# Performance work log

Measured on AMD Instinct MI355X. Metric: run time of the kernel, lower is better.

## Reference

```python
import jax, jax.numpy as jnp
import numpy as np

B, T, D, H = 4, 2048, 1024, 16
HD = D // H

def setup_inputs() -> dict:
    key = jax.random.key(0)
    ks = jax.random.split(key, 5)
    s = 0.02
    return {
        "x": jax.random.normal(ks[0], (B, T, D), dtype=jnp.float32),
        "w_qkv": jax.random.normal(ks[1], (D, 3 * D), dtype=jnp.float32) * s,
        "b_qkv": jax.random.normal(ks[2], (3 * D,), dtype=jnp.float32) * s,
        "w_proj": jax.random.normal(ks[3], (D, D), dtype=jnp.float32) * s,
        "b_proj": jax.random.normal(ks[4], (D,), dtype=jnp.float32) * s,
    }

def reference(x, w_qkv, b_qkv, w_proj, b_proj):
    b, t, c = x.shape
    h, hd = H, HD
    scale = hd ** -0.5
    qkv = x @ w_qkv + b_qkv                       # [B,T,3D]
    qkv = qkv.reshape(b, t, 3, h, hd)
    q, k, v = qkv[:, :, 0], qkv[:, :, 1], qkv[:, :, 2]   # [B,T,H,HD]
    # scores [B,H,T,T]
    att = jnp.einsum('bqhd,bkhd->bhqk', q, k) * scale
    causal = jnp.tril(jnp.ones((t, t), dtype=bool))
    att = jnp.where(causal[None, None], att, -jnp.inf)
    w = jax.nn.softmax(att, axis=-1)
    out = jnp.einsum('bhqk,bkhd->bqhd', w, v).reshape(b, t, c)
    return out @ w_proj + b_proj
```

## Files before the change

### kernel.cpp

```cpp
#include <hip/hip_runtime.h>
#include <hip/hip_bf16.h>
#include <cstdint>

#define BB 4
#define TT 2048
#define DD 1024
#define HH 16
#define HD 64
#define MM (BB*TT)
#define NQKV (3*DD)
#define QSCALE 0.18033688f
#define NQT 16

typedef __bf16 bf16;
typedef __bf16 bf16x8 __attribute__((ext_vector_type(8)));
typedef float f32x4 __attribute__((ext_vector_type(4)));

#define AS1 __attribute__((address_space(1)))
#define AS3 __attribute__((address_space(3)))

__device__ __forceinline__ void gload_lds16(const void* g, void* l) {
  __builtin_amdgcn_global_load_lds((const AS1 uint32_t*)g, (AS3 uint32_t*)l, 16, 0, 0);
}

__global__ void k_cvt_x(const float* __restrict__ in, bf16* __restrict__ out) {
  int i = blockIdx.x * blockDim.x + threadIdx.x;
  float4 v = ((const float4*)in)[i];
  ushort4 o;
  o.x = __builtin_bit_cast(unsigned short, (bf16)v.x);
  o.y = __builtin_bit_cast(unsigned short, (bf16)v.y);
  o.z = __builtin_bit_cast(unsigned short, (bf16)v.z);
  o.w = __builtin_bit_cast(unsigned short, (bf16)v.w);
  ((ushort4*)out)[i] = o;
}

__global__ void k_transpose_w(const float* __restrict__ in, bf16* __restrict__ out,
                              int R, int C) {
  __shared__ float tile[32][33];
  const int c0 = blockIdx.x * 32, r0 = blockIdx.y * 32;
  const int tx = threadIdx.x & 31, ty = threadIdx.x >> 5;
#pragma unroll
  for (int i = 0; i < 32; i += 8)
    tile[ty + i][tx] = in[(long)(r0 + ty + i) * C + c0 + tx];
  __syncthreads();
#pragma unroll
  for (int i = 0; i < 32; i += 8)
    out[(long)(c0 + ty + i) * R + r0 + tx] = (bf16)tile[tx][ty + i];
}

__global__ void k_transpose_v(const bf16* __restrict__ V, bf16* __restrict__ Vt) {
  __shared__ bf16 tile[64][65];
  const int bh = blockIdx.z;
  const int t0 = blockIdx.x * 64;
  const bf16* src = V + (long)bh * TT * HD;
  bf16* dst = Vt + (long)bh * HD * TT;
  const int tx = threadIdx.x & 63, ty = threadIdx.x >> 6;
#pragma unroll
  for (int i = 0; i < 64; i += 4)
    tile[ty + i][tx] = src[(long)(t0 + ty + i) * HD + tx];
  __syncthreads();
#pragma unroll
  for (int i = 0; i < 64; i += 4)
    dst[(long)(ty + i) * TT + t0 + tx] = tile[tx][ty + i];
}

template <int EPI>
__global__ __launch_bounds__(256) void k_gemm(
    const bf16* __restrict__ A, const bf16* __restrict__ Bt,
    const float* __restrict__ bias, float* __restrict__ fout,
    bf16* __restrict__ q_out, bf16* __restrict__ k_out, bf16* __restrict__ v_out,
    int K) {
  __shared__ bf16 sm[2 * 128 * 64];
  bf16* const As = sm;
  bf16* const Bs = sm + 128 * 64;
  const int tid = threadIdx.x;
  const int m0 = blockIdx.x * 128;
  const int n0 = blockIdx.y * 128;
  const int wv = tid >> 6, lane = tid & 63;
  const int g = lane >> 4, lr = lane & 15;
  const int wm = (wv >> 1) * 64, wn = (wv & 1) * 64;
  const int sr = tid >> 3, sc = tid & 7;
  f32x4 acc[4][4] = {};

  for (int k0 = 0; k0 < K; k0 += 64) {
#pragma unroll
    for (int p = 0; p < 4; ++p) {
      const int row = p * 32 + sr;
      const int chunk = sc ^ (row & 7);
      gload_lds16(A + ((long)(m0 + row) * K + k0 + (chunk << 3)),
                  As + (row << 6) + (sc << 3));
      gload_lds16(Bt + ((long)(n0 + row) * K + k0 + (chunk << 3)),
                  Bs + (row << 6) + (sc << 3));
    }
    __syncthreads();
#pragma unroll
    for (int kf = 0; kf < 2; ++kf) {
      bf16x8 af[4], bfr[4];
#pragma unroll
      for (int mf = 0; mf < 4; ++mf) {
        const int row = wm + mf * 16 + lr;
        af[mf] = *(const bf16x8*)((const char*)As +
                 (((row << 7) + (kf << 6) + (g << 4)) ^ ((row & 7) << 4)));
      }
#pragma unroll
      for (int nf = 0; nf < 4; ++nf) {
        const int row = wn + nf * 16 + lr;
        bfr[nf] = *(const bf16x8*)((const char*)Bs +
                 (((row << 7) + (kf << 6) + (g << 4)) ^ ((row & 7) << 4)));
      }
#pragma unroll
      for (int mf = 0; mf < 4; ++mf)
#pragma unroll
        for (int nf = 0; nf < 4; ++nf)
          acc[mf][nf] = __builtin_amdgcn_mfma_f32_16x16x32_bf16(af[mf], bfr[nf],
                                                                acc[mf][nf], 0, 0, 0);
    }
    __syncthreads();
  }

  if (EPI == 0) {
    const int sel = n0 >> 10;
    const int d0 = n0 & 1023;
    const float qs = (sel == 0) ? QSCALE : 1.0f;
    bf16* Cs = sm;
#pragma unroll
    for (int nf = 0; nf < 4; ++nf) {
      const int col = wn + nf * 16 + lr;
      const float bv = bias[n0 + col];
#pragma unroll
      for (int mf = 0; mf < 4; ++mf)
#pragma unroll
        for (int j = 0; j < 4; ++j) {
          const int row = wm + mf * 16 + g * 4 + j;
          const float v = (acc[mf][nf][j] + bv) * qs;
          const int cp = (col >> 3) ^ (((row >> 2) & 3) << 1);
          Cs[(row << 7) + (cp << 3) + (col & 7)] = (bf16)v;
        }
    }
    __syncthreads();
    bf16* dst = (sel == 0) ? q_out : (sel == 1 ? k_out : v_out);
    const int b = m0 >> 11;
    const int t0 = m0 & 2047;
    const int h0 = d0 >> 6;
#pragma unroll
    for (int i = 0; i < 8; ++i) {
      const int cid = (i << 8) + tid;
      const int hh = cid >> 10;
      const int r  = (cid >> 3) & 127;
      const int ck = cid & 7;
      const int cp = ((hh << 3) + ck) ^ (((r >> 2) & 3) << 1);
      const bf16x8 vv = *(const bf16x8*)&Cs[(r << 7) + (cp << 3)];
      const long off = ((((long)b * HH + h0 + hh) * TT + t0 + r) << 6) + (ck << 3);
      *(bf16x8*)(dst + off) = vv;
    }
  } else {
    float* Cf = (float*)sm;
#pragma unroll
    for (int pass = 0; pass < 2; ++pass) {
      __syncthreads();
      if ((wm >> 6) == pass) {
#pragma unroll
        for (int nf = 0; nf < 4; ++nf) {
          const int col = wn + nf * 16 + lr;
          const float bv = bias[n0 + col];
#pragma unroll
          for (int mf = 0; mf < 4; ++mf)
#pragma unroll
            for (int j = 0; j < 4; ++j) {
              const int row = mf * 16 + g * 4 + j;
              const int cp = (col >> 2) ^ (((row >> 2) & 3) << 1);
              Cf[(row << 7) + (cp << 2) + (col & 3)] = acc[mf][nf][j] + bv;
            }
        }
      }
      __syncthreads();
#pragma unroll
      for (int i = 0; i < 8; ++i) {
        const int cid = (i << 8) + tid;
        const int r  = cid >> 5;
        const int ck = cid & 31;
        const int cp = ck ^ (((r >> 2) & 3) << 1);
        const float4 vv = *(const float4*)&Cf[(r << 7) + (cp << 2)];
        const long rowm = m0 + (pass << 6) + r;
        *(float4*)&fout[rowm * DD + n0 + (ck << 2)] = vv;
      }
    }
  }
}

template <bool MASKED>
__device__ __forceinline__ void attn_tile(
    const bf16* __restrict__ Kt, const bf16* __restrict__ Vt,
    bf16* __restrict__ Pw, const bf16x8 (&qf)[2][2],
    f32x4 (&acc)[2][4], f32x4 (&ls)[2],
    int rowbase, int kv0, int g, int lr, bf16x8 ones) {
  f32x4 s[2][4] = {};
#pragma unroll
  for (int kf = 0; kf < 2; ++kf) {
    bf16x8 bfr[4];
#pragma unroll
    for (int nf = 0; nf < 4; ++nf) {
      const int row = nf * 16 + lr;
      bfr[nf] = *(const bf16x8*)((const char*)Kt +
               (((row << 7) + (kf << 6) + (g << 4)) ^ ((row & 7) << 4)));
    }
#pragma unroll
    for (int mf = 0; mf < 2; ++mf)
#pragma unroll
      for (int nf = 0; nf < 4; ++nf)
        s[mf][nf] = __builtin_amdgcn_mfma_f32_16x16x32_bf16(qf[mf][kf], bfr[nf],
                                                            s[mf][nf], 0, 0, 0);
  }
#pragma unroll
  for (int mf = 0; mf < 2; ++mf) {
#pragma unroll
    for (int nf = 0; nf < 4; ++nf) {
      const int col = kv0 + nf * 16 + lr;
#pragma unroll
      for (int j = 0; j < 4; ++j) {
        float p;
        if (MASKED) {
          const int rowq = rowbase + mf * 16 + g * 4 + j;
          p = (col <= rowq) ? __builtin_amdgcn_exp2f(s[mf][nf][j]) : 0.f;
        } else {
          p = __builtin_amdgcn_exp2f(s[mf][nf][j]);
        }
        const int prow = mf * 16 + g * 4 + j;
        const int pcol = nf * 16 + lr;
        *(bf16*)((char*)Pw +
                 (((prow << 7) + (pcol << 1)) ^ ((prow & 7) << 4))) = (bf16)p;
      }
    }
  }
#pragma unroll
  for (int kf = 0; kf < 2; ++kf) {
    bf16x8 pa[2], vb[4];
#pragma unroll
    for (int mf = 0; mf < 2; ++mf) {
      const int row = mf * 16 + lr;
      pa[mf] = *(const bf16x8*)((const char*)Pw +
               (((row << 7) + (kf << 6) + (g << 4)) ^ ((row & 7) << 4)));
    }
#pragma unroll
    for (int nf = 0; nf < 4; ++nf) {
      const int row = nf * 16 + lr;
      vb[nf] = *(const bf16x8*)((const char*)Vt +
               (((row << 7) + (kf << 6) + (g << 4)) ^ ((row & 7) << 4)));
    }
#pragma unroll
    for (int mf = 0; mf < 2; ++mf)
      ls[mf] = __builtin_amdgcn_mfma_f32_16x16x32_bf16(pa[mf], ones, ls[mf], 0, 0, 0);
#pragma unroll
    for (int mf = 0; mf < 2; ++mf)
#pragma unroll
      for (int nf = 0; nf < 4; ++nf)
        acc[mf][nf] = __builtin_amdgcn_mfma_f32_16x16x32_bf16(pa[mf], vb[nf],
                                                              acc[mf][nf], 0, 0, 0);
  }
}

__global__ __launch_bounds__(256, 2) void k_attn(
    const bf16* __restrict__ Q, const bf16* __restrict__ K,
    const bf16* __restrict__ Vt, bf16* __restrict__ O) {
  __shared__ bf16 Ks[2][64 * 64];
  __shared__ bf16 Vs[2][64 * 64];
  __shared__ bf16 Ps[4][32 * 64];
  const int tid = threadIdx.x;
  const int qa = blockIdx.x, qb = NQT - 1 - qa;
  const int bh = blockIdx.y;
  const int b = bh >> 4, h = bh & 15;
  const int wv = tid >> 6, lane = tid & 63;
  const int g = lane >> 4, lr = lane & 15;
  const int ra = qa * 128 + wv * 32;
  const int rb = qb * 128 + wv * 32;
  const bf16* Qb = Q + (long)bh * TT * HD;
  const bf16* Kb = K + (long)bh * TT * HD;
  const bf16* Vb = Vt + (long)bh * HD * TT;
  bf16* Pw = &Ps[wv][0];

  bf16x8 ones;
#pragma unroll
  for (int i = 0; i < 8; ++i) ones[i] = (bf16)1.0f;

  bf16x8 qfa[2][2], qfb[2][2];
#pragma unroll
  for (int mf = 0; mf < 2; ++mf)
#pragma unroll
    for (int kf = 0; kf < 2; ++kf) {
      qfa[mf][kf] = *(const bf16x8*)(Qb + ((long)(ra + mf * 16 + lr) << 6) +
                                     kf * 32 + g * 8);
      qfb[mf][kf] = *(const bf16x8*)(Qb + ((long)(rb + mf * 16 + lr) << 6) +
                                     kf * 32 + g * 8);
    }

  f32x4 acca[2][4] = {}, accb[2][4] = {};
  f32x4 lsa[2] = {}, lsb[2] = {};

  const int sr = tid >> 3, sc = tid & 7;
  const int nkv = 2 * qb + 2;

  auto STAGE = [&](int buf, int kt) {
    const int kv0 = kt * 64;
#pragma unroll
    for (int p = 0; p < 2; ++p) {
      const int row = p * 32 + sr;
      const int chunk = sc ^ (row & 7);
      gload_lds16(Kb + ((long)(kv0 + row) << 6) + (chunk << 3),
                  &Ks[buf][(row << 6) + (sc << 3)]);
      gload_lds16(Vb + (long)row * TT + kv0 + (chunk << 3),
                  &Vs[buf][(row << 6) + (sc << 3)]);
    }
  };

  STAGE(0, 0);
  __syncthreads();

  int cur = 0;
  for (int kt = 0; kt < nkv; ++kt) {
    const int kv0 = kt * 64;
    if (kt + 1 < nkv) STAGE(cur ^ 1, kt + 1);

    const bf16* Kt  = &Ks[cur][0];
    const bf16* Vtl = &Vs[cur][0];
    if (kv0 + 63 <= ra)
      attn_tile<false>(Kt, Vtl, Pw, qfa, acca, lsa, ra, kv0, g, lr, ones);
    else if (kv0 <= ra + 31)
      attn_tile<true >(Kt, Vtl, Pw, qfa, acca, lsa, ra, kv0, g, lr, ones);
    if (kv0 + 63 <= rb)
      attn_tile<false>(Kt, Vtl, Pw, qfb, accb, lsb, rb, kv0, g, lr, ones);
    else if (kv0 <= rb + 31)
      attn_tile<true >(Kt, Vtl, Pw, qfb, accb, lsb, rb, kv0, g, lr, ones);

    __syncthreads();
    cur ^= 1;
  }

#pragma unroll
  for (int mf = 0; mf < 2; ++mf) {
    float inva[4], invb[4];
#pragma unroll
    for (int j = 0; j < 4; ++j) {
      inva[j] = 1.0f / lsa[mf][j];
      invb[j] = 1.0f / lsb[mf][j];
    }
#pragma unroll
    for (int nf = 0; nf < 4; ++nf) {
      const int col = h * 64 + nf * 16 + lr;
#pragma unroll
      for (int j = 0; j < 4; ++j) {
        const int ta = ra + mf * 16 + g * 4 + j;
        const int tb = rb + mf * 16 + g * 4 + j;
        O[(((long)b * TT + ta) << 10) + col] = (bf16)(acca[mf][nf][j] * inva[j]);
        O[(((long)b * TT + tb) << 10) + col] = (bf16)(accb[mf][nf][j] * invb[j]);
      }
    }
  }
}

extern "C" void kernel_launch(void* const* d_in, const int* in_sizes, int n_in,
                              void* d_out, int out_size, void* d_ws, size_t ws_size,
                              hipStream_t stream) {
  (void)in_sizes; (void)n_in; (void)out_size; (void)ws_size;
  const float* x      = (const float*)d_in[0];
  const float* w_qkv  = (const float*)d_in[1];
  const float* b_qkv  = (const float*)d_in[2];
  const float* w_proj = (const float*)d_in[3];
  const float* b_proj = (const float*)d_in[4];
  float* out = (float*)d_out;

  bf16* ws = (bf16*)d_ws;
  const long NX = (long)MM * DD;
  bf16* xb     = ws;
  bf16* wqkvT  = xb + NX;
  bf16* wprojT = wqkvT + (long)NQKV * DD;
  bf16* Qb     = wprojT + (long)DD * DD;
  bf16* Kb     = Qb + NX;
  bf16* Vb     = Kb + NX;
  bf16* Vtb    = xb;
  bf16* attout = Vb;

  k_cvt_x<<<(int)(NX / 4 / 256), 256, 0, stream>>>(x, xb);
  k_transpose_w<<<dim3(NQKV / 32, DD / 32), 256, 0, stream>>>(w_qkv, wqkvT, DD, NQKV);
  k_transpose_w<<<dim3(DD / 32, DD / 32), 256, 0, stream>>>(w_proj, wprojT, DD, DD);
  k_gemm<0><<<dim3(MM / 128, NQKV / 128), 256, 0, stream>>>(
      xb, wqkvT, b_qkv, nullptr, Qb, Kb, Vb, DD);
  k_transpose_v<<<dim3(TT / 64, 1, BB * HH), 256, 0, stream>>>(Vb, Vtb);
  k_attn<<<dim3(NQT / 2, BB * HH), 256, 0, stream>>>(Qb, Kb, Vtb, attout);
  k_gemm<1><<<dim3(MM / 128, DD / 128), 256, 0, stream>>>(
      attout, wprojT, b_proj, out, nullptr, nullptr, nullptr, DD);
}
```

Before: 180.9 us.

## Rewrite attention tile with 32x32 MFMA, register-resident P, one q-tile per block

Moves the attention inner tile from 16x16x32 MFMAs to 32x32x16 MFMAs and computes S transposed (K as the A operand), so P stays in registers. P is packed to bf16 and exchanged between wave halves with ds_bpermute instead of going through an LDS scratch buffer. The paired q-tile load balancing (qa plus its mirror qb per block) is dropped: each block now handles a single q-tile, and the grid doubles with reverse ordering so the longest blocks launch first. This removes the LDS P round trip and halves the MFMA instruction count, but it gives up the balanced work per block and halves K/V reuse per staged tile.

```diff
diff --git a/kernel.cpp b/kernel.cpp
--- a/kernel.cpp
+++ b/kernel.cpp
@@ -15,12 +15,20 @@
 typedef __bf16 bf16;
 typedef __bf16 bf16x8 __attribute__((ext_vector_type(8)));
 typedef float f32x4 __attribute__((ext_vector_type(4)));
+typedef float f32x16 __attribute__((ext_vector_type(16)));
+typedef int i32x4 __attribute__((ext_vector_type(4)));
 
 #define AS1 __attribute__((address_space(1)))
 #define AS3 __attribute__((address_space(3)))
 
 __device__ __forceinline__ void gload_lds16(const void* g, void* l) {
   __builtin_amdgcn_global_load_lds((const AS1 uint32_t*)g, (AS3 uint32_t*)l, 16, 0, 0);
+}
+
+__device__ __forceinline__ int pack2bf16(float lo, float hi) {
+  unsigned a = __builtin_bit_cast(unsigned short, (bf16)lo);
+  unsigned b = __builtin_bit_cast(unsigned short, (bf16)hi);
+  return (int)(a | (b << 16));
 }
 
 __global__ void k_cvt_x(const float* __restrict__ in, bf16* __restrict__ out) {
@@ -189,73 +197,68 @@
 }
 
 template <bool MASKED>
-__device__ __forceinline__ void attn_tile(
-    const bf16* __restrict__ Kt, const bf16* __restrict__ Vt,
-    bf16* __restrict__ Pw, const bf16x8 (&qf)[2][2],
-    f32x4 (&acc)[2][4], f32x4 (&ls)[2],
-    int rowbase, int kv0, int g, int lr, bf16x8 ones) {
-  f32x4 s[2][4] = {};
-#pragma unroll
-  for (int kf = 0; kf < 2; ++kf) {
-    bf16x8 bfr[4];
-#pragma unroll
-    for (int nf = 0; nf < 4; ++nf) {
-      const int row = nf * 16 + lr;
-      bfr[nf] = *(const bf16x8*)((const char*)Kt +
-               (((row << 7) + (kf << 6) + (g << 4)) ^ ((row & 7) << 4)));
-    }
-#pragma unroll
-    for (int mf = 0; mf < 2; ++mf)
-#pragma unroll
-      for (int nf = 0; nf < 4; ++nf)
-        s[mf][nf] = __builtin_amdgcn_mfma_f32_16x16x32_bf16(qf[mf][kf], bfr[nf],
-                                                            s[mf][nf], 0, 0, 0);
-  }
-#pragma unroll
-  for (int mf = 0; mf < 2; ++mf) {
-#pragma unroll
-    for (int nf = 0; nf < 4; ++nf) {
-      const int col = kv0 + nf * 16 + lr;
-#pragma unroll
-      for (int j = 0; j < 4; ++j) {
-        float p;
-        if (MASKED) {
-          const int rowq = rowbase + mf * 16 + g * 4 + j;
-          p = (col <= rowq) ? __builtin_amdgcn_exp2f(s[mf][nf][j]) : 0.f;
-        } else {
-          p = __builtin_amdgcn_exp2f(s[mf][nf][j]);
-        }
-        const int prow = mf * 16 + g * 4 + j;
-        const int pcol = nf * 16 + lr;
-        *(bf16*)((char*)Pw +
-                 (((prow << 7) + (pcol << 1)) ^ ((prow & 7) << 4))) = (bf16)p;
-      }
-    }
-  }
-#pragma unroll
-  for (int kf = 0; kf < 2; ++kf) {
-    bf16x8 pa[2], vb[4];
-#pragma unroll
-    for (int mf = 0; mf < 2; ++mf) {
-      const int row = mf * 16 + lr;
-      pa[mf] = *(const bf16x8*)((const char*)Pw +
-               (((row << 7) + (kf << 6) + (g << 4)) ^ ((row & 7) << 4)));
-    }
-#pragma unroll
-    for (int nf = 0; nf < 4; ++nf) {
-      const int row = nf * 16 + lr;
-      vb[nf] = *(const bf16x8*)((const char*)Vt +
-               (((row << 7) + (kf << 6) + (g << 4)) ^ ((row & 7) << 4)));
-    }
-#pragma unroll
-    for (int mf = 0; mf < 2; ++mf)
-      ls[mf] = __builtin_amdgcn_mfma_f32_16x16x32_bf16(pa[mf], ones, ls[mf], 0, 0, 0);
-#pragma unroll
-    for (int mf = 0; mf < 2; ++mf)
-#pragma unroll
-      for (int nf = 0; nf < 4; ++nf)
-        acc[mf][nf] = __builtin_amdgcn_mfma_f32_16x16x32_bf16(pa[mf], vb[nf],
-                                                              acc[mf][nf], 0, 0, 0);
+__device__ __forceinline__ void attn_tile32(
+    const bf16* __restrict__ Kt, const bf16* __restrict__ Vtl,
+    const bf16x8 (&qf)[4], f32x16 (&acc)[2], f32x16 &ls,
+    int rowbase, int kv0, int lane, int xaddr, bf16x8 ones) {
+  const int l31 = lane & 31;
+  const int hf  = lane >> 5;
+  f32x16 st0 = {}, st1 = {};
+#pragma unroll
+  for (int kf = 0; kf < 4; ++kf) {
+    const int colb = kf * 32 + hf * 16;
+    const int r0 = l31, r1 = 32 + l31;
+    bf16x8 k0 = *(const bf16x8*)((const char*)Kt + (((r0 << 7) + colb) ^ ((r0 & 7) << 4)));
+    bf16x8 k1 = *(const bf16x8*)((const char*)Kt + (((r1 << 7) + colb) ^ ((r1 & 7) << 4)));
+    st0 = __builtin_amdgcn_mfma_f32_32x32x16_bf16(k0, qf[kf], st0, 0, 0, 0);
+    st1 = __builtin_amdgcn_mfma_f32_32x32x16_bf16(k1, qf[kf], st1, 0, 0, 0);
+  }
+  const int q = rowbase + l31;
+  const int kvb = kv0 + 4 * hf;
+  int pk0[8], pk1[8];
+#pragma unroll
+  for (int c = 0; c < 8; ++c) {
+    const int off = 2 * (c & 1) + 8 * (c >> 1);
+    float p00 = __builtin_amdgcn_exp2f(st0[2 * c]);
+    float p01 = __builtin_amdgcn_exp2f(st0[2 * c + 1]);
+    float p10 = __builtin_amdgcn_exp2f(st1[2 * c]);
+    float p11 = __builtin_amdgcn_exp2f(st1[2 * c + 1]);
+    if (MASKED) {
+      if (kvb + off > q)          p00 = 0.f;
+      if (kvb + off + 1 > q)      p01 = 0.f;
+      if (kvb + 32 + off > q)     p10 = 0.f;
+      if (kvb + 32 + off + 1 > q) p11 = 0.f;
+    }
+    pk0[c] = pack2bf16(p00, p01);
+    pk1[c] = pack2bf16(p10, p11);
+  }
+  int pq0[8], pq1[8];
+#pragma unroll
+  for (int c = 0; c < 8; ++c) {
+    pq0[c] = __builtin_amdgcn_ds_bpermute(xaddr, pk0[c]);
+    pq1[c] = __builtin_amdgcn_ds_bpermute(xaddr, pk1[c]);
+  }
+  const bool hi = (hf == 1);
+#pragma unroll
+  for (int kpos = 0; kpos < 4; ++kpos) {
+    const int* PK = (kpos < 2) ? pk0 : pk1;
+    const int* PQ = (kpos < 2) ? pq0 : pq1;
+    i32x4 w;
+#pragma unroll
+    for (int t = 0; t < 4; ++t) {
+      const int cA = 4 * (kpos & 1) + (t & 1);
+      const int cB = cA + 2;
+      w[t] = ((t >> 1) == 0) ? (hi ? PQ[cB] : PK[cA])
+                             : (hi ? PK[cB] : PQ[cA]);
+    }
+    const bf16x8 paf = __builtin_bit_cast(bf16x8, w);
+    const int vcolb = kpos * 32 + hf * 16;
+    const int vr0 = l31, vr1 = 32 + l31;
+    bf16x8 v0 = *(const bf16x8*)((const char*)Vtl + (((vr0 << 7) + vcolb) ^ ((vr0 & 7) << 4)));
+    bf16x8 v1 = *(const bf16x8*)((const char*)Vtl + (((vr1 << 7) + vcolb) ^ ((vr1 & 7) << 4)));
+    acc[0] = __builtin_amdgcn_mfma_f32_32x32x16_bf16(paf, v0, acc[0], 0, 0, 0);
+    acc[1] = __builtin_amdgcn_mfma_f32_32x32x16_bf16(paf, v1, acc[1], 0, 0, 0);
+    ls = __builtin_amdgcn_mfma_f32_32x32x16_bf16(paf, ones, ls, 0, 0, 0);
   }
 }
 
@@ -264,40 +267,33 @@
     const bf16* __restrict__ Vt, bf16* __restrict__ O) {
   __shared__ bf16 Ks[2][64 * 64];
   __shared__ bf16 Vs[2][64 * 64];
-  __shared__ bf16 Ps[4][32 * 64];
   const int tid = threadIdx.x;
-  const int qa = blockIdx.x, qb = NQT - 1 - qa;
+  const int qa = NQT - 1 - blockIdx.x;
   const int bh = blockIdx.y;
   const int b = bh >> 4, h = bh & 15;
   const int wv = tid >> 6, lane = tid & 63;
-  const int g = lane >> 4, lr = lane & 15;
+  const int l31 = lane & 31, hf = lane >> 5;
   const int ra = qa * 128 + wv * 32;
-  const int rb = qb * 128 + wv * 32;
   const bf16* Qb = Q + (long)bh * TT * HD;
   const bf16* Kb = K + (long)bh * TT * HD;
   const bf16* Vb = Vt + (long)bh * HD * TT;
-  bf16* Pw = &Ps[wv][0];
+  const int xaddr = (lane ^ 32) << 2;
 
   bf16x8 ones;
 #pragma unroll
   for (int i = 0; i < 8; ++i) ones[i] = (bf16)1.0f;
 
-  bf16x8 qfa[2][2], qfb[2][2];
-#pragma unroll
-  for (int mf = 0; mf < 2; ++mf)
-#pragma unroll
-    for (int kf = 0; kf < 2; ++kf) {
-      qfa[mf][kf] = *(const bf16x8*)(Qb + ((long)(ra + mf * 16 + lr) << 6) +
-                                     kf * 32 + g * 8);
-      qfb[mf][kf] = *(const bf16x8*)(Qb + ((long)(rb + mf * 16 + lr) << 6) +
-                                     kf * 32 + g * 8);
-    }
-
-  f32x4 acca[2][4] = {}, accb[2][4] = {};
-  f32x4 lsa[2] = {}, lsb[2] = {};
+  bf16x8 qf[4];
+  {
+    const bf16* qrow = Qb + ((long)(ra + l31) << 6) + hf * 8;
+#pragma unroll
+    for (int kf = 0; kf < 4; ++kf) qf[kf] = *(const bf16x8*)(qrow + kf * 16);
+  }
+
+  f32x16 acc[2] = {}, ls = {};
 
   const int sr = tid >> 3, sc = tid & 7;
-  const int nkv = 2 * qb + 2;
+  const int nkv = 2 * qa + 2;
 
   auto STAGE = [&](int buf, int kt) {
     const int kv0 = kt * 64;
@@ -320,40 +316,23 @@
     const int kv0 = kt * 64;
     if (kt + 1 < nkv) STAGE(cur ^ 1, kt + 1);
 
-    const bf16* Kt  = &Ks[cur][0];
-    const bf16* Vtl = &Vs[cur][0];
     if (kv0 + 63 <= ra)
-      attn_tile<false>(Kt, Vtl, Pw, qfa, acca, lsa, ra, kv0, g, lr, ones);
+      attn_tile32<false>(&Ks[cur][0], &Vs[cur][0], qf, acc, ls, ra, kv0, lane, xaddr, ones);
     else if (kv0 <= ra + 31)
-      attn_tile<true >(Kt, Vtl, Pw, qfa, acca, lsa, ra, kv0, g, lr, ones);
-    if (kv0 + 63 <= rb)
-      attn_tile<false>(Kt, Vtl, Pw, qfb, accb, lsb, rb, kv0, g, lr, ones);
-    else if (kv0 <= rb + 31)
-      attn_tile<true >(Kt, Vtl, Pw, qfb, accb, lsb, rb, kv0, g, lr, ones);
+      attn_tile32<true >(&Ks[cur][0], &Vs[cur][0], qf, acc, ls, ra, kv0, lane, xaddr, ones);
 
     __syncthreads();
     cur ^= 1;
   }
 
-#pragma unroll
-  for (int mf = 0; mf < 2; ++mf) {
-    float inva[4], invb[4];
-#pragma unroll
-    for (int j = 0; j < 4; ++j) {
-      inva[j] = 1.0f / lsa[mf][j];
-      invb[j] = 1.0f / lsb[mf][j];
-    }
-#pragma unroll
-    for (int nf = 0; nf < 4; ++nf) {
-      const int col = h * 64 + nf * 16 + lr;
-#pragma unroll
-      for (int j = 0; j < 4; ++j) {
-        const int ta = ra + mf * 16 + g * 4 + j;
-        const int tb = rb + mf * 16 + g * 4 + j;
-        O[(((long)b * TT + ta) << 10) + col] = (bf16)(acca[mf][nf][j] * inva[j]);
-        O[(((long)b * TT + tb) << 10) + col] = (bf16)(accb[mf][nf][j] * invb[j]);
-      }
-    }
+  const int colb = h * 64 + l31;
+#pragma unroll
+  for (int j = 0; j < 16; ++j) {
+    const int trow = ra + (j & 3) + 8 * (j >> 2) + 4 * hf;
+    const float inv = 1.0f / ls[j];
+    const long base = ((long)b * TT + trow) << 10;
+    O[base + colb]      = (bf16)(acc[0][j] * inv);
+    O[base + colb + 32] = (bf16)(acc[1][j] * inv);
   }
 }
 
@@ -385,7 +364,7 @@
   k_gemm<0><<<dim3(MM / 128, NQKV / 128), 256, 0, stream>>>(
       xb, wqkvT, b_qkv, nullptr, Qb, Kb, Vb, DD);
   k_transpose_v<<<dim3(TT / 64, 1, BB * HH), 256, 0, stream>>>(Vb, Vtb);
-  k_attn<<<dim3(NQT / 2, BB * HH), 256, 0, stream>>>(Qb, Kb, Vtb, attout);
+  k_attn<<<dim3(NQT, BB * HH), 256, 0, stream>>>(Qb, Kb, Vtb, attout);
   k_gemm<1><<<dim3(MM / 128, DD / 128), 256, 0, stream>>>(
       attout, wprojT, b_proj, out, nullptr, nullptr, nullptr, DD);
 }
```

New measurement: 217.8 us. +20.3%, slower.
